# Performance work log

Measured on AMD Instinct MI355X. Metric: run time of the kernel, lower is better.

## Reference

```python
import jax, jax.numpy as jnp
import numpy as np

HIDDEN = 1024
ATT_FEAT = 2048
EMBED = 512


def setup_inputs() -> dict:
    key = jax.random.key(0)
    k1, k2, k3, k4, k5, k6 = jax.random.split(key, 6)
    B, S, N = 16, 64, 196
    hidden = jax.random.normal(k1, (B, S, HIDDEN), dtype=jnp.float32)
    feats = jax.random.normal(k2, (B, N, ATT_FEAT), dtype=jnp.float32)
    att_mask = jax.random.randint(k3, (B, N), 0, 2, dtype=jnp.int32)
    # parameters (scaled like default torch Linear init)
    w_h = jax.random.normal(k4, (HIDDEN, EMBED), dtype=jnp.float32) / np.sqrt(HIDDEN)
    w_u = jax.random.normal(k5, (ATT_FEAT, EMBED), dtype=jnp.float32) / np.sqrt(ATT_FEAT)
    b = jnp.ones((EMBED,), dtype=jnp.float32)
    w = jax.random.normal(k6, (EMBED,), dtype=jnp.float32) / np.sqrt(EMBED)
    return {"hidden": hidden, "feats": feats, "att_mask": att_mask,
            "w_h": w_h, "w_u": w_u, "b": b, "w": w}


def reference(hidden, feats, att_mask, w_h, w_u, b, w):
    # hidden: [B,S,H], feats: [B,N,F], att_mask: [B,N]
    Wh = jnp.einsum('bsh,he->bse', hidden, w_h)          # [B,S,E]
    Uv = jnp.einsum('bnf,fe->bne', feats, w_u)           # [B,N,E] (feats repeat is redundant; same math)
    # additive attention energies: tanh(Wh + Uv + b) . w  -> [B,S,N]
    e = jnp.tanh(Wh[:, :, None, :] + Uv[:, None, :, :] + b)
    scores = jnp.einsum('bsne,e->bsn', e, w)             # [B,S,N]
    scores = jnp.where(att_mask[:, None, :] == 0, jnp.float32(-1e9), scores)
    weights = jax.nn.softmax(scores, axis=-1)            # [B,S,N]
    attn_feats = jnp.einsum('bsn,bnf->bsf', weights, feats)  # [B,S,F]
    return attn_feats, weights
```

## Files before the change

kernel.cpp:

```cpp
#include <hip/hip_runtime.h>
#include <math.h>

#define BATCH 16
#define SEQ 64
#define NKEY 196
#define HIDDEN 1024
#define ATT_FEAT 2048
#define EMBED 512
#define MPAD 3200

using half8    = __attribute__((ext_vector_type(8))) _Float16;
using f32x4    = __attribute__((ext_vector_type(4))) float;
using f32x16   = __attribute__((ext_vector_type(16))) float;
using float4v  = __attribute__((ext_vector_type(4))) float;

#define KCONST (-2.8853900817779268f)
#define LOG2E  (1.4426950408889634f)

__device__ __forceinline__ void gl_lds16(const _Float16* g, _Float16* l) {
    __builtin_amdgcn_global_load_lds(
        (const __attribute__((address_space(1))) unsigned int*)g,
        (__attribute__((address_space(3))) unsigned int*)l, 16, 0, 0);
}

__device__ inline void prep_a128(
    const float* __restrict__ A, _Float16* __restrict__ T,
    int K, int Mreal, int tm, int tk, int t)
{
    const int r  = t >> 1;
    const int hf = t & 1;
    const int grow = tm * 128 + r;
    float f[32];
    if (grow < Mreal) {
        const float* src = A + (size_t)grow * K + tk * 64 + hf * 32;
        #pragma unroll
        for (int q = 0; q < 8; ++q) {
            float4v v = *(const float4v*)(src + q * 4);
            f[q*4+0] = v.x; f[q*4+1] = v.y; f[q*4+2] = v.z; f[q*4+3] = v.w;
        }
    } else {
        #pragma unroll
        for (int j = 0; j < 32; ++j) f[j] = 0.f;
    }
    const int tkk = tk * 2 + hf;
    const size_t base = ((size_t)tm * (K >> 5) + tkk) * 4096;
    #pragma unroll
    for (int s = 0; s < 2; ++s)
        #pragma unroll
        for (int kh = 0; kh < 2; ++kh) {
            half8 h;
            #pragma unroll
            for (int j = 0; j < 8; ++j)
                h[j] = (_Float16)f[s * 16 + kh * 8 + j];
            *(half8*)(T + base + (size_t)((s * 2 + kh) * 128 + r) * 8) = h;
        }
}

__device__ inline void prep_b128(
    const float* __restrict__ W, _Float16* __restrict__ T,
    int K, int N, int tn, int tk, int t, float (*tile)[129])
{
    {
        const int kr = t >> 2;
        const int nc = (t & 3) * 32;
        const float* src = W + (size_t)(tk * 64 + kr) * N + tn * 128 + nc;
        #pragma unroll
        for (int q = 0; q < 8; ++q) {
            float4v v = *(const float4v*)(src + q * 4);
            tile[kr][nc + q*4 + 0] = v.x; tile[kr][nc + q*4 + 1] = v.y;
            tile[kr][nc + q*4 + 2] = v.z; tile[kr][nc + q*4 + 3] = v.w;
        }
    }
    __syncthreads();
    {
        const int c  = t >> 1;
        const int hf = t & 1;
        const int tkk = tk * 2 + hf;
        const size_t base = ((size_t)tn * (K >> 5) + tkk) * 4096;
        #pragma unroll
        for (int s = 0; s < 2; ++s)
            #pragma unroll
            for (int kh = 0; kh < 2; ++kh) {
                half8 h;
                #pragma unroll
                for (int j = 0; j < 8; ++j)
                    h[j] = (_Float16)tile[hf * 32 + s * 16 + kh * 8 + j][c];
                *(half8*)(T + base + (size_t)((s * 2 + kh) * 128 + c) * 8) = h;
            }
    }
}

__global__ __launch_bounds__(256) void uber_prep(
    const float* __restrict__ hidden, const float* __restrict__ feats,
    const float* __restrict__ w_h, const float* __restrict__ w_u,
    _Float16* HA, _Float16* FA, _Float16* HB, _Float16* UB)
{
    __shared__ float tile[64][129];
    const int id = blockIdx.x;
    const int t  = threadIdx.x;
    if (id < 128) {
        prep_a128(hidden, HA, HIDDEN, BATCH * SEQ, id >> 4, id & 15, t);
    } else if (id < 928) {
        const int j = id - 128;
        prep_a128(feats, FA, ATT_FEAT, BATCH * NKEY, j >> 5, j & 31, t);
    } else if (id < 992) {
        const int j = id - 928;
        prep_b128(w_h, HB, HIDDEN, EMBED, j >> 4, j & 15, t, tile);
    } else {
        const int j = id - 992;
        prep_b128(w_u, UB, ATT_FEAT, EMBED, j >> 5, j & 31, t, tile);
    }
}

__global__ __launch_bounds__(256) void uber_gemm(
    const _Float16* __restrict__ HA, const _Float16* __restrict__ HB,
    const _Float16* __restrict__ FA, const _Float16* __restrict__ UB,
    const float* __restrict__ bvec, float* __restrict__ WhP, float* __restrict__ UvP)
{
    __shared__ __align__(16) _Float16 L[2][4][4096];

    const int hh = blockIdx.x;
    const int t0 = (hh & 7) * 58 + (hh >> 3);

    const _Float16 *Aimg, *Bimg;
    const float* bias = nullptr;
    float* C;
    int rt, ct, tk0, aK;
    if (t0 < 400) {
        const int ks = t0 / 100, rem = t0 % 100;
        rt = rem >> 2; ct = rem & 3;
        Aimg = FA; Bimg = UB;
        aK = ATT_FEAT >> 5; tk0 = ks * 16;
        C = UvP + (size_t)ks * MPAD * EMBED;
        if (ks == 0) bias = bvec;
    } else {
        const int v = t0 - 400;
        const int ks = v >> 5, rem = v & 31;
        rt = rem >> 2; ct = rem & 3;
        Aimg = HA; Bimg = HB;
        aK = HIDDEN >> 5; tk0 = ks * 16;
        C = WhP + (size_t)ks * (BATCH * SEQ) * EMBED;
    }

    const int tid = threadIdx.x, lane = tid & 63, w = tid >> 6;
    const int wr = w >> 1, wc = w & 1;
    const int l31 = lane & 31, kh = lane >> 5;

    const int isB = w >> 1;
    const int whf = w & 1;
    const _Float16* srcMat = isB ? Bimg : Aimg;
    const int majorTile = isB ? ct : rt;
    const _Float16* src0 =
        srcMat + ((size_t)majorTile * aK + tk0) * 4096 + whf * 2048 + lane * 8;

    f32x16 acc[2][2] = {};

    auto stage = [&](int buf, int t) {
        const _Float16* s = src0 + (size_t)t * 4096;
        _Float16* d = &L[isB][buf][0] + whf * 2048 + lane * 8;
        #pragma unroll
        for (int c = 0; c < 4; ++c)
            gl_lds16(s + c * 512, d + c * 512);
    };

    auto compute = [&](int buf) {
        #pragma unroll
        for (int s = 0; s < 2; ++s) {
            const int rb = (s * 2 + kh) * 128;
            half8 a[2], b[2];
            #pragma unroll
            for (int m = 0; m < 2; ++m)
                a[m] = *(const half8*)&L[0][buf][(rb + wr * 64 + m * 32 + l31) * 8];
            #pragma unroll
            for (int n = 0; n < 2; ++n)
                b[n] = *(const half8*)&L[1][buf][(rb + wc * 64 + n * 32 + l31) * 8];
            __builtin_amdgcn_s_setprio(1);
            #pragma unroll
            for (int m = 0; m < 2; ++m)
                #pragma unroll
                for (int n = 0; n < 2; ++n)
                    acc[m][n] = __builtin_amdgcn_mfma_f32_32x32x16_f16(a[m], b[n], acc[m][n], 0, 0, 0);
            __builtin_amdgcn_s_setprio(0);
        }
    };

    stage(0, 0); stage(1, 1); stage(2, 2);
    #pragma unroll 1
    for (int t = 0; t < 16; ++t) {
        if (t + 2 < 16)      asm volatile("s_waitcnt vmcnt(8)" ::: "memory");
        else if (t + 1 < 16) asm volatile("s_waitcnt vmcnt(4)" ::: "memory");
        else                 asm volatile("s_waitcnt vmcnt(0)" ::: "memory");
        __builtin_amdgcn_s_barrier();
        if (t + 3 < 16) stage((t + 3) & 3, t + 3);
        __builtin_amdgcn_sched_barrier(0);
        compute(t & 3);
        __builtin_amdgcn_sched_barrier(0);
    }

    #pragma unroll
    for (int m = 0; m < 2; ++m) {
        const int row0 = rt * 128 + wr * 64 + m * 32;
        #pragma unroll
        for (int n = 0; n < 2; ++n) {
            const int colg = ct * 128 + wc * 64 + n * 32 + l31;
            const float bv = bias ? bias[colg] : 0.f;
            #pragma unroll
            for (int r = 0; r < 16; ++r) {
                const int row = (r & 3) + 8 * (r >> 2) + 4 * kh;
                C[(size_t)(row0 + row) * EMBED + colg] = (acc[m][n][r] + bv) * KCONST;
            }
        }
    }
}

__global__ __launch_bounds__(256) void scores4_kernel(
    const float* __restrict__ WhP, const float* __restrict__ UvP,
    const float* __restrict__ wvec, float* __restrict__ scr4)
{
    const int n0 = blockIdx.x * 16;
    const int eq = blockIdx.y;
    const int b  = blockIdx.z;
    const int tid = threadIdx.x;
    const int w    = tid >> 6;
    const int lane = tid & 63;

    __shared__ float whs[64 * 64];
    __shared__ float uvs[16][64];

    const size_t WHS = (size_t)(BATCH * SEQ) * EMBED;
    const size_t UVS = (size_t)MPAD * EMBED;

    float acc[4] = {};
    char* whsB = (char*)whs;

    for (int ch = 0; ch < 2; ++ch) {
        const int e0 = eq * 128 + ch * 64;
        {
            const int r = tid >> 2;
            const float* Wr = WhP + (size_t)(b * SEQ + r) * EMBED + e0;
            #pragma unroll
            for (int q = 0; q < 4; ++q) {
                const int cc = (tid & 3) * 16 + q * 4;
                float4v v = *(const float4v*)(Wr + cc)
                          + *(const float4v*)(Wr + WHS + cc);
                *(float4v*)(whsB + r * 256 + ((cc * 4) ^ ((r & 15) << 4))) = v;
            }
        }
        {
            const int nl = tid >> 4;
            const int c4 = tid & 15;
            const int nr = (n0 + nl < NKEY) ? (n0 + nl) : (NKEY - 1);
            const float* Ur = UvP + (size_t)(b * NKEY + nr) * EMBED + e0 + c4 * 4;
            float4v u = *(const float4v*)(Ur)
                      + *(const float4v*)(Ur + UVS)
                      + *(const float4v*)(Ur + 2 * UVS)
                      + *(const float4v*)(Ur + 3 * UVS);
            *(float4v*)&uvs[nl][c4 * 4] = u;
        }
        __syncthreads();

        #pragma unroll
        for (int ec = 0; ec < 8; ++ec) {
            const int sb = lane * 256;
            float4v wh0 = *(const float4v*)(whsB + sb + ((ec * 32 +  0) ^ ((lane & 15) << 4)));
            float4v wh1 = *(const float4v*)(whsB + sb + ((ec * 32 + 16) ^ ((lane & 15) << 4)));
            float wf[8];
            #pragma unroll
            for (int i = 0; i < 8; ++i) wf[i] = wvec[e0 + ec * 8 + i];
            #pragma unroll
            for (int j = 0; j < 4; ++j) {
                const int nl = w * 4 + j;
                float4v u0 = *(const float4v*)&uvs[nl][ec * 8];
                float4v u1 = *(const float4v*)&uvs[nl][ec * 8 + 4];
                float t0 = __builtin_amdgcn_exp2f(wh0.x + u0.x);
                float t1 = __builtin_amdgcn_exp2f(wh0.y + u0.y);
                float t2 = __builtin_amdgcn_exp2f(wh0.z + u0.z);
                float t3 = __builtin_amdgcn_exp2f(wh0.w + u0.w);
                float t4 = __builtin_amdgcn_exp2f(wh1.x + u1.x);
                float t5 = __builtin_amdgcn_exp2f(wh1.y + u1.y);
                float t6 = __builtin_amdgcn_exp2f(wh1.z + u1.z);
                float t7 = __builtin_amdgcn_exp2f(wh1.w + u1.w);
                float a = acc[j];
                a = fmaf(wf[0], __builtin_amdgcn_rcpf(1.f + t0), a);
                a = fmaf(wf[1], __builtin_amdgcn_rcpf(1.f + t1), a);
                a = fmaf(wf[2], __builtin_amdgcn_rcpf(1.f + t2), a);
                a = fmaf(wf[3], __builtin_amdgcn_rcpf(1.f + t3), a);
                a = fmaf(wf[4], __builtin_amdgcn_rcpf(1.f + t4), a);
                a = fmaf(wf[5], __builtin_amdgcn_rcpf(1.f + t5), a);
                a = fmaf(wf[6], __builtin_amdgcn_rcpf(1.f + t6), a);
                a = fmaf(wf[7], __builtin_amdgcn_rcpf(1.f + t7), a);
                acc[j] = a;
            }
        }
        __syncthreads();
    }

    float* dst = scr4 + ((size_t)eq * (BATCH * SEQ) + b * SEQ + lane) * NKEY;
    #pragma unroll
    for (int j = 0; j < 4; ++j) {
        const int n = n0 + w * 4 + j;
        if (n < NKEY) dst[n] = 2.f * acc[j];
    }
}

__global__ __launch_bounds__(256) void attn_softmax_kernel(
    const float* __restrict__ scr4, const int* __restrict__ mask,
    const float* __restrict__ feats,
    float* __restrict__ weights_out, float* __restrict__ out)
{
    const int t   = threadIdx.x;
    const int fb  = blockIdx.x;
    const int s0  = blockIdx.y * 4;
    const int b   = blockIdx.z;

    __shared__ float wt[NKEY][4];

    const size_t SCRS = (size_t)(BATCH * SEQ) * NKEY;

    {
        const int r  = t >> 6;
        const int ln = t & 63;
        const float* p = scr4 + (size_t)(b * SEQ + s0 + r) * NKEY;
        const int* mrow = mask + b * NKEY;
        float v[4];
        float mx = -INFINITY;
        #pragma unroll
        for (int j = 0; j < 4; ++j) {
            const int n = ln + 64 * j;
            float s = -INFINITY;
            if (n < NKEY) {
                s = p[n] + p[SCRS + n] + p[2 * SCRS + n] + p[3 * SCRS + n];
                if (mrow[n] == 0) s = -1e9f;
            }
            v[j] = s;
            mx = fmaxf(mx, s);
        }
        #pragma unroll
        for (int off = 32; off; off >>= 1) mx = fmaxf(mx, __shfl_xor(mx, off));
        float sum = 0.f;
        #pragma unroll
        for (int j = 0; j < 4; ++j) {
            v[j] = __builtin_amdgcn_exp2f((v[j] - mx) * LOG2E);
            if (ln + 64 * j < NKEY) sum += v[j];
        }
        #pragma unroll
        for (int off = 32; off; off >>= 1) sum += __shfl_xor(sum, off);
        const float inv = __builtin_amdgcn_rcpf(sum);
        float* wrow = weights_out + (size_t)(b * SEQ + s0 + r) * NKEY;
        #pragma unroll
        for (int j = 0; j < 4; ++j) {
            const int n = ln + 64 * j;
            if (n < NKEY) {
                const float wv = v[j] * inv;
                wt[n][r] = wv;
                if (fb == 0) wrow[n] = wv;
            }
        }
    }
    __syncthreads();

    const int col = fb * 1024 + t * 4;
    const float* fp = feats + (size_t)b * NKEY * ATT_FEAT + col;

    float4v acc[4] = {};
    #pragma unroll 4
    for (int n = 0; n < NKEY; ++n) {
        float4v f  = *(const float4v*)(fp + (size_t)n * ATT_FEAT);
        float4v wv = *(const float4v*)&wt[n][0];
        acc[0] += wv.x * f;
        acc[1] += wv.y * f;
        acc[2] += wv.z * f;
        acc[3] += wv.w * f;
    }

    float* op = out + (size_t)(b * SEQ + s0) * ATT_FEAT + col;
    #pragma unroll
    for (int s = 0; s < 4; ++s)
        *(float4v*)(op + (size_t)s * ATT_FEAT) = acc[s];
}

extern "C" void kernel_launch(void* const* d_in, const int* in_sizes, int n_in,
                              void* d_out, int out_size, void* d_ws, size_t ws_size,
                              hipStream_t stream)
{
    const float* hidden = (const float*)d_in[0];
    const float* feats  = (const float*)d_in[1];
    const int*   mask   = (const int*)  d_in[2];
    const float* w_h    = (const float*)d_in[3];
    const float* w_u    = (const float*)d_in[4];
    const float* bvec   = (const float*)d_in[5];
    const float* wvec   = (const float*)d_in[6];

    float* out         = (float*)d_out;
    float* attn_out    = out;
    float* weights_out = out + (size_t)BATCH * SEQ * ATT_FEAT;

    float* WhP  = (float*)d_ws;
    float* UvP  = WhP + (size_t)2 * BATCH * SEQ * EMBED;
    float* scr4 = UvP + (size_t)4 * MPAD * EMBED;
    _Float16* FA = (_Float16*)(scr4 + (size_t)4 * BATCH * SEQ * NKEY);
    _Float16* HA = FA + (size_t)MPAD * ATT_FEAT;
    _Float16* UB = HA + (size_t)BATCH * SEQ * HIDDEN;
    _Float16* HB = UB + (size_t)EMBED * ATT_FEAT;

    uber_prep<<<dim3(1120), 256, 0, stream>>>(
        hidden, feats, w_h, w_u, HA, FA, HB, UB);

    uber_gemm<<<dim3(464), 256, 0, stream>>>(
        HA, HB, FA, UB, bvec, WhP, UvP);

    scores4_kernel<<<dim3((NKEY + 15) / 16, 4, BATCH), 256, 0, stream>>>(
        WhP, UvP, wvec, scr4);

    attn_softmax_kernel<<<dim3(2, SEQ / 4, BATCH), 256, 0, stream>>>(
        scr4, mask, feats, weights_out, attn_out);
}
```

Before: 88.60 us.

## Store GEMM partials in fp16 and process 8 rows per attention block

The split-K partial outputs of the projection GEMM (Wh and Uv partials) are now written as fp16 instead of fp32. The scores kernel reads and sums them in fp32, which roughly halves the traffic between the two kernels. The final attention kernel now handles 8 sequence rows per block instead of 4, so each feats element loaded is reused across twice as many rows and the grid halves. The trade-off is lower precision in the intermediate energies and higher register pressure from 8 float4 accumulators.

```diff
diff --git a/kernel.cpp b/kernel.cpp
--- a/kernel.cpp
+++ b/kernel.cpp
@@ -10,6 +10,7 @@
 #define MPAD 3200
 
 using half8    = __attribute__((ext_vector_type(8))) _Float16;
+using half4    = __attribute__((ext_vector_type(4))) _Float16;
 using f32x4    = __attribute__((ext_vector_type(4))) float;
 using f32x16   = __attribute__((ext_vector_type(16))) float;
 using float4v  = __attribute__((ext_vector_type(4))) float;
@@ -115,7 +116,8 @@
 __global__ __launch_bounds__(256) void uber_gemm(
     const _Float16* __restrict__ HA, const _Float16* __restrict__ HB,
     const _Float16* __restrict__ FA, const _Float16* __restrict__ UB,
-    const float* __restrict__ bvec, float* __restrict__ WhP, float* __restrict__ UvP)
+    const float* __restrict__ bvec, _Float16* __restrict__ WhP,
+    _Float16* __restrict__ UvP)
 {
     __shared__ __align__(16) _Float16 L[2][4][4096];
 
@@ -124,7 +126,7 @@
 
     const _Float16 *Aimg, *Bimg;
     const float* bias = nullptr;
-    float* C;
+    _Float16* C;
     int rt, ct, tk0, aK;
     if (t0 < 400) {
         const int ks = t0 / 100, rem = t0 % 100;
@@ -207,14 +209,15 @@
             #pragma unroll
             for (int r = 0; r < 16; ++r) {
                 const int row = (r & 3) + 8 * (r >> 2) + 4 * kh;
-                C[(size_t)(row0 + row) * EMBED + colg] = (acc[m][n][r] + bv) * KCONST;
+                C[(size_t)(row0 + row) * EMBED + colg] =
+                    (_Float16)((acc[m][n][r] + bv) * KCONST);
             }
         }
     }
 }
 
 __global__ __launch_bounds__(256) void scores4_kernel(
-    const float* __restrict__ WhP, const float* __restrict__ UvP,
+    const _Float16* __restrict__ WhP, const _Float16* __restrict__ UvP,
     const float* __restrict__ wvec, float* __restrict__ scr4)
 {
     const int n0 = blockIdx.x * 16;
@@ -237,12 +240,21 @@
         const int e0 = eq * 128 + ch * 64;
         {
             const int r = tid >> 2;
-            const float* Wr = WhP + (size_t)(b * SEQ + r) * EMBED + e0;
+            const _Float16* Wr = WhP + (size_t)(b * SEQ + r) * EMBED + e0 + (tid & 3) * 16;
+            half8 h0 = *(const half8*)(Wr);
+            half8 h1 = *(const half8*)(Wr + 8);
+            half8 g0 = *(const half8*)(Wr + WHS);
+            half8 g1 = *(const half8*)(Wr + WHS + 8);
+            float f[16];
+            #pragma unroll
+            for (int j = 0; j < 8; ++j) {
+                f[j]     = (float)h0[j] + (float)g0[j];
+                f[8 + j] = (float)h1[j] + (float)g1[j];
+            }
             #pragma unroll
             for (int q = 0; q < 4; ++q) {
                 const int cc = (tid & 3) * 16 + q * 4;
-                float4v v = *(const float4v*)(Wr + cc)
-                          + *(const float4v*)(Wr + WHS + cc);
+                float4v v = { f[q*4+0], f[q*4+1], f[q*4+2], f[q*4+3] };
                 *(float4v*)(whsB + r * 256 + ((cc * 4) ^ ((r & 15) << 4))) = v;
             }
         }
@@ -250,11 +262,16 @@
             const int nl = tid >> 4;
             const int c4 = tid & 15;
             const int nr = (n0 + nl < NKEY) ? (n0 + nl) : (NKEY - 1);
-            const float* Ur = UvP + (size_t)(b * NKEY + nr) * EMBED + e0 + c4 * 4;
-            float4v u = *(const float4v*)(Ur)
-                      + *(const float4v*)(Ur + UVS)
-                      + *(const float4v*)(Ur + 2 * UVS)
-                      + *(const float4v*)(Ur + 3 * UVS);
+            const _Float16* Ur = UvP + (size_t)(b * NKEY + nr) * EMBED + e0 + c4 * 4;
+            half4 u0 = *(const half4*)(Ur);
+            half4 u1 = *(const half4*)(Ur + UVS);
+            half4 u2 = *(const half4*)(Ur + 2 * UVS);
+            half4 u3 = *(const half4*)(Ur + 3 * UVS);
+            float4v u;
+            u.x = ((float)u0[0] + (float)u1[0]) + ((float)u2[0] + (float)u3[0]);
+            u.y = ((float)u0[1] + (float)u1[1]) + ((float)u2[1] + (float)u3[1]);
+            u.z = ((float)u0[2] + (float)u1[2]) + ((float)u2[2] + (float)u3[2]);
+            u.w = ((float)u0[3] + (float)u1[3]) + ((float)u2[3] + (float)u3[3]);
             *(float4v*)&uvs[nl][c4 * 4] = u;
         }
         __syncthreads();
@@ -310,46 +327,46 @@
 {
     const int t   = threadIdx.x;
     const int fb  = blockIdx.x;
-    const int s0  = blockIdx.y * 4;
+    const int s0  = blockIdx.y * 8;
     const int b   = blockIdx.z;
 
-    __shared__ float wt[NKEY][4];
+    __shared__ float wt[NKEY][8];
 
     const size_t SCRS = (size_t)(BATCH * SEQ) * NKEY;
 
     {
-        const int r  = t >> 6;
-        const int ln = t & 63;
+        const int r  = t >> 5;
+        const int ln = t & 31;
         const float* p = scr4 + (size_t)(b * SEQ + s0 + r) * NKEY;
         const int* mrow = mask + b * NKEY;
-        float v[4];
+        float v[7];
         float mx = -INFINITY;
         #pragma unroll
-        for (int j = 0; j < 4; ++j) {
-            const int n = ln + 64 * j;
+        for (int j = 0; j < 7; ++j) {
+            const int n = ln + 32 * j;
             float s = -INFINITY;
             if (n < NKEY) {
-                s = p[n] + p[SCRS + n] + p[2 * SCRS + n] + p[3 * SCRS + n];
+                s = (p[n] + p[SCRS + n]) + (p[2 * SCRS + n] + p[3 * SCRS + n]);
                 if (mrow[n] == 0) s = -1e9f;
             }
             v[j] = s;
             mx = fmaxf(mx, s);
         }
         #pragma unroll
-        for (int off = 32; off; off >>= 1) mx = fmaxf(mx, __shfl_xor(mx, off));
+        for (int off = 16; off; off >>= 1) mx = fmaxf(mx, __shfl_xor(mx, off));
         float sum = 0.f;
         #pragma unroll
-        for (int j = 0; j < 4; ++j) {
+        for (int j = 0; j < 7; ++j) {
             v[j] = __builtin_amdgcn_exp2f((v[j] - mx) * LOG2E);
-            if (ln + 64 * j < NKEY) sum += v[j];
-        }
-        #pragma unroll
-        for (int off = 32; off; off >>= 1) sum += __shfl_xor(sum, off);
+            if (ln + 32 * j < NKEY) sum += v[j];
+        }
+        #pragma unroll
+        for (int off = 16; off; off >>= 1) sum += __shfl_xor(sum, off);
         const float inv = __builtin_amdgcn_rcpf(sum);
         float* wrow = weights_out + (size_t)(b * SEQ + s0 + r) * NKEY;
         #pragma unroll
-        for (int j = 0; j < 4; ++j) {
-            const int n = ln + 64 * j;
+        for (int j = 0; j < 7; ++j) {
+            const int n = ln + 32 * j;
             if (n < NKEY) {
                 const float wv = v[j] * inv;
                 wt[n][r] = wv;
@@ -362,20 +379,25 @@
     const int col = fb * 1024 + t * 4;
     const float* fp = feats + (size_t)b * NKEY * ATT_FEAT + col;
 
-    float4v acc[4] = {};
+    float4v acc[8] = {};
     #pragma unroll 4
     for (int n = 0; n < NKEY; ++n) {
         float4v f  = *(const float4v*)(fp + (size_t)n * ATT_FEAT);
-        float4v wv = *(const float4v*)&wt[n][0];
-        acc[0] += wv.x * f;
-        acc[1] += wv.y * f;
-        acc[2] += wv.z * f;
-        acc[3] += wv.w * f;
+        float4v w0 = *(const float4v*)&wt[n][0];
+        float4v w1 = *(const float4v*)&wt[n][4];
+        acc[0] += w0.x * f;
+        acc[1] += w0.y * f;
+        acc[2] += w0.z * f;
+        acc[3] += w0.w * f;
+        acc[4] += w1.x * f;
+        acc[5] += w1.y * f;
+        acc[6] += w1.z * f;
+        acc[7] += w1.w * f;
     }
 
     float* op = out + (size_t)(b * SEQ + s0) * ATT_FEAT + col;
     #pragma unroll
-    for (int s = 0; s < 4; ++s)
+    for (int s = 0; s < 8; ++s)
         *(float4v*)(op + (size_t)s * ATT_FEAT) = acc[s];
 }
 
@@ -395,9 +417,9 @@
     float* attn_out    = out;
     float* weights_out = out + (size_t)BATCH * SEQ * ATT_FEAT;
 
-    float* WhP  = (float*)d_ws;
-    float* UvP  = WhP + (size_t)2 * BATCH * SEQ * EMBED;
-    float* scr4 = UvP + (size_t)4 * MPAD * EMBED;
+    _Float16* WhP = (_Float16*)d_ws;
+    _Float16* UvP = WhP + (size_t)2 * BATCH * SEQ * EMBED;
+    float*    scr4 = (float*)(UvP + (size_t)4 * MPAD * EMBED);
     _Float16* FA = (_Float16*)(scr4 + (size_t)4 * BATCH * SEQ * NKEY);
     _Float16* HA = FA + (size_t)MPAD * ATT_FEAT;
     _Float16* UB = HA + (size_t)BATCH * SEQ * HIDDEN;
@@ -412,6 +434,6 @@
     scores4_kernel<<<dim3((NKEY + 15) / 16, 4, BATCH), 256, 0, stream>>>(
         WhP, UvP, wvec, scr4);
 
-    attn_softmax_kernel<<<dim3(2, SEQ / 4, BATCH), 256, 0, stream>>>(
+    attn_softmax_kernel<<<dim3(2, SEQ / 8, BATCH), 256, 0, stream>>>(
         scr4, mask, feats, weights_out, attn_out);
 }
```

New measurement: 89.17 us. No clear change (+0.6%).
